# Kernel tuning notes

Hardware: AMD Instinct MI355X
Metric: run time of the kernel (lower is better)

Reference implementation:

```python
import jax, jax.numpy as jnp
import numpy as np


def setup_inputs() -> dict:
    key = jax.random.key(0)
    ks = jax.random.split(key, 9)
    B, S, D, DK, DV = 4, 4096, 1024, 128, 128
    scale = 1.0 / np.sqrt(D)
    return {
        "q": jax.random.normal(ks[0], (B, S, D), jnp.float32),
        "k": jax.random.normal(ks[1], (B, S, D), jnp.float32),
        "v": jax.random.normal(ks[2], (B, S, D), jnp.float32),
        "Wq": jax.random.normal(ks[3], (D, DK), jnp.float32) * scale,
        "bq": jnp.zeros((DK,), jnp.float32),
        "Wk": jax.random.normal(ks[4], (D, DK), jnp.float32) * scale,
        "bk": jnp.zeros((DK,), jnp.float32),
        "Wv": jax.random.normal(ks[5], (D, DV), jnp.float32) * scale,
        "bv": jnp.zeros((DV,), jnp.float32),
    }


def reference(q, k, v, Wq, bq, Wk, bk, Wv, bv):
    # Q/K/V projections (nn.Linear)
    Q = q @ Wq + bq          # [B,S,DK]
    K = k @ Wk + bk          # [B,S,DK]
    V = v @ Wv + bv          # [B,S,DV]
    scale = Q.shape[-1] ** 0.5
    scores = jnp.einsum("bqd,bkd->bqk", Q, K) / scale  # [B,Sq,Sk]
    attn = jax.nn.softmax(scores, axis=-1)
    return jnp.einsum("bqk,bkd->bqd", attn, V)          # [B,Sq,DV]
```

## Files before the change

### kernel.cpp

```cpp
#include <hip/hip_runtime.h>
#include <hip/hip_bf16.h>
#include <cstdint>
#include <cmath>


typedef __bf16 bf16x8 __attribute__((ext_vector_type(8)));
typedef float f32x4 __attribute__((ext_vector_type(4)));
typedef float f32x16 __attribute__((ext_vector_type(16)));

typedef const __attribute__((address_space(1))) unsigned int* gp_t;
typedef __attribute__((address_space(3))) unsigned int* lp_t;

__device__ __forceinline__ unsigned short f2bf(float f) {
  unsigned u = __float_as_uint(f);
  u += 0x7fffu + ((u >> 16) & 1u);
  return (unsigned short)(u >> 16);
}

__device__ __forceinline__ bf16x8 ld_frag(const char* p) {
  uint4 u = *reinterpret_cast<const uint4*>(p);
  return __builtin_bit_cast(bf16x8, u);
}

__device__ __forceinline__ unsigned cvtpk_bf16(float lo, float hi) {
  unsigned r;
  asm("v_cvt_pk_bf16_f32 %0, %1, %2" : "=v"(r) : "v"(lo), "v"(hi));
  return r;
}

__device__ __forceinline__ void pl32swap(unsigned &a, unsigned &b) {
  asm("v_permlane32_swap_b32 %0, %1" : "+v"(a), "+v"(b));
}

__device__ __forceinline__ bf16x8 mk_frag(unsigned w0, unsigned w1, unsigned w2, unsigned w3) {
  uint4 u{w0, w1, w2, w3};
  return __builtin_bit_cast(bf16x8, u);
}

__device__ __forceinline__ float bfhi2f(unsigned u) {
  return __uint_as_float(u & 0xffff0000u);
}
__device__ __forceinline__ float bflo2f(unsigned u) {
  return __uint_as_float(u << 16);
}

#define QSCALE_LOG2E 0.12751744f

__global__ __launch_bounds__(256) void prep_wt_kernel(
    const float* __restrict__ W0, const float* __restrict__ W1, const float* __restrict__ W2,
    unsigned short* __restrict__ T0, unsigned short* __restrict__ T1,
    unsigned short* __restrict__ T2) {
  const int mode = blockIdx.z;
  const float* W = (mode == 0) ? W0 : (mode == 1) ? W1 : W2;
  unsigned short* Wt = (mode == 0) ? T0 : (mode == 1) ? T1 : T2;
  __shared__ float tile[64][65];
  int kt = blockIdx.x, nt = blockIdx.y;
  int tid = threadIdx.x;
  int c = tid & 63;
  int r0 = (tid >> 6) * 16;
#pragma unroll
  for (int i = 0; i < 16; ++i) {
    int r = r0 + i;
    tile[r][c] = W[(size_t)(kt * 64 + r) * 128 + nt * 64 + c];
  }
  __syncthreads();
#pragma unroll
  for (int i = 0; i < 16; ++i) {
    int n = r0 + i;
    Wt[(size_t)(nt * 64 + n) * 1024 + kt * 64 + c] = f2bf(tile[c][n]);
  }
}

__global__ __launch_bounds__(256, 3) void proj_kernel(
    const float* __restrict__ qx, const float* __restrict__ kx, const float* __restrict__ vx,
    const unsigned short* __restrict__ Wtq, const unsigned short* __restrict__ Wtk,
    const unsigned short* __restrict__ Wtv,
    const float* __restrict__ bq, const float* __restrict__ bk, const float* __restrict__ bv,
    unsigned short* __restrict__ Qb, unsigned short* __restrict__ Kb,
    unsigned short* __restrict__ Vtb) {
  const int mode = blockIdx.y;
  const float* x = (mode == 0) ? qx : (mode == 1) ? kx : vx;
  const unsigned short* Wt = (mode == 0) ? Wtq : (mode == 1) ? Wtk : Wtv;
  const float* bias = (mode == 0) ? bq : (mode == 1) ? bk : bv;

  __shared__ __align__(16) char lds[49152];
  char* ldsA = lds;
  char* ldsW = lds + 16384;

  const int tid = threadIdx.x;
  const int lane = tid & 63, wid = tid >> 6;
  const int l15 = lane & 15, hi = lane >> 4;
  const long row0 = (long)blockIdx.x * 64;

  const int a_row0 = tid >> 5;
  const int a_c16  = tid & 31;
  const float* a_src = x + (row0 + a_row0) * 1024 + a_c16 * 4;
  const int a_swz = (a_row0 & 7) << 4;
  const int a_wbyte = (((a_c16 >> 1) * 16) ^ a_swz) + (a_c16 & 1) * 8;

  const char* w_src = (const char*)Wt + (size_t)(tid >> 4) * 2048 +
                      (size_t)((tid & 15) ^ ((tid >> 4) & 7)) * 16;

  f32x4 acc[8];
#pragma unroll
  for (int i = 0; i < 8; ++i) acc[i] = f32x4{0.f, 0.f, 0.f, 0.f};

  const int arow = wid * 16 + l15;
  const int aswzr = (arow & 7) << 4;

#pragma unroll 1
  for (int t = 0; t < 8; ++t) {
    f32x4 av[8];
#pragma unroll
    for (int j = 0; j < 8; ++j)
      av[j] = *reinterpret_cast<const f32x4*>(a_src + t * 128 + j * 8192);
#pragma unroll
    for (int i = 0; i < 8; ++i)
      __builtin_amdgcn_global_load_lds((gp_t)(w_src + (size_t)i * 32768 + t * 256),
                                       (lp_t)(ldsW + i * 4096 + wid * 1024), 16, 0, 0);
#pragma unroll
    for (int j = 0; j < 8; ++j) {
      uint2 wv;
      wv.x = cvtpk_bf16(av[j][0], av[j][1]);
      wv.y = cvtpk_bf16(av[j][2], av[j][3]);
      *reinterpret_cast<uint2*>(ldsA + a_row0 * 256 + j * 2048 + a_wbyte) = wv;
    }
    __syncthreads();

    bf16x8 af[4];
#pragma unroll
    for (int kk = 0; kk < 4; ++kk)
      af[kk] = ld_frag(ldsA + ((arow * 256 + (kk * 4 + hi) * 16) ^ aswzr));
#pragma unroll
    for (int ni = 0; ni < 8; ++ni) {
      int n = ni * 16 + l15;
      int nswz = (n & 7) << 4;
#pragma unroll
      for (int kk = 0; kk < 4; ++kk) {
        bf16x8 wf = ld_frag(ldsW + ((n * 256 + (kk * 4 + hi) * 16) ^ nswz));
        acc[ni] = __builtin_amdgcn_mfma_f32_16x16x32_bf16(af[kk], wf, acc[ni], 0, 0, 0);
      }
    }
    __syncthreads();
  }

#pragma unroll
  for (int ni = 0; ni < 8; ++ni) {
    int n = ni * 16 + l15;
    float bv_ = bias[n];
    long m = row0 + wid * 16 + hi * 4;
    f32x4 a = acc[ni];
    if (mode == 2) {
      int bb = (int)(m >> 12);
      int s = (int)(m & 4095);
      ushort4 pk;
      pk.x = f2bf(a[0] + bv_); pk.y = f2bf(a[1] + bv_);
      pk.z = f2bf(a[2] + bv_); pk.w = f2bf(a[3] + bv_);
      *reinterpret_cast<ushort4*>(Vtb + ((size_t)(bb * 128 + n)) * 4096 + s) = pk;
    } else {
      const float sc = (mode == 0) ? QSCALE_LOG2E : 1.0f;
      unsigned short* outp = (mode == 0) ? Qb : Kb;
      outp[(m + 0) * 128 + n] = f2bf((a[0] + bv_) * sc);
      outp[(m + 1) * 128 + n] = f2bf((a[1] + bv_) * sc);
      outp[(m + 2) * 128 + n] = f2bf((a[2] + bv_) * sc);
      outp[(m + 3) * 128 + n] = f2bf((a[3] + bv_) * sc);
    }
  }
}

template <int TPS>
__global__ __launch_bounds__(256, 2) void attn_kernel(
    const unsigned short* __restrict__ Qb, const unsigned short* __restrict__ Kb,
    const unsigned short* __restrict__ Vtb, unsigned short* __restrict__ Po,
    float* __restrict__ ml) {
  __shared__ __align__(16) char lds[65536];

  const int tid = threadIdx.x;
  const int lane = tid & 63, wid = tid >> 6;
  const int l31 = lane & 31, hi = lane >> 5;
  const int split = blockIdx.y;
  const int b = blockIdx.z;
  const int qbase = blockIdx.x * 128 + wid * 32;
  const size_t growq = (size_t)b * 4096 + qbase + l31;

  const char* kg0 = (const char*)Kb + (size_t)(b * 4096) * 256;
  const char* vg0 = (const char*)Vtb + (size_t)b * 128 * 4096 * 2;
  const int k_row = tid >> 4;
  const int slog  = (tid & 15) ^ (tid >> 4);
  const int v_dv0 = 2 * (tid >> 4) + (slog >> 3);
  const int v_ksl = slog & 7;

#define ATTN_STAGE(KV0, BUF)                                                          \
  {                                                                                   \
    char* kb_ = lds + (BUF) * 16384;                                                  \
    char* vb_ = lds + 32768 + (BUF) * 16384;                                          \
    const char* kgs_ = kg0 + (size_t)(KV0) * 256 + (size_t)k_row * 256 + slog * 16;   \
    const char* vgs_ = vg0 + (size_t)(KV0) * 2 + (size_t)v_dv0 * 8192 + v_ksl * 16;   \
    _Pragma("unroll")                                                                 \
    for (int i = 0; i < 4; ++i)                                                       \
      __builtin_amdgcn_global_load_lds((gp_t)(kgs_ + (size_t)i * 4096),               \
                                       (lp_t)(kb_ + i * 4096 + wid * 1024), 16, 0, 0);\
    _Pragma("unroll")                                                                 \
    for (int i = 0; i < 4; ++i)                                                       \
      __builtin_amdgcn_global_load_lds((gp_t)(vgs_ + (size_t)i * 262144),             \
                                       (lp_t)(vb_ + i * 4096 + wid * 1024), 16, 0, 0);\
  }

  bf16x8 qf[8];
  {
    const unsigned short* qp = Qb + growq * 128 + hi * 8;
#pragma unroll
    for (int kt = 0; kt < 8; ++kt)
      qf[kt] = __builtin_bit_cast(bf16x8, *reinterpret_cast<const uint4*>(qp + kt * 16));
  }

  f32x16 oacc[4];
#pragma unroll
  for (int d = 0; d < 4; ++d)
#pragma unroll
    for (int j = 0; j < 16; ++j) oacc[d][j] = 0.f;
  float mrun = -INFINITY, lrun = 0.f;

  const int t0 = split * TPS, t1 = t0 + TPS;

  ATTN_STAGE(t0 * 64, 0);
  ATTN_STAGE((t0 + 1) * 64, 1);

  const int kswz = l31 & 15;
  const int vjx  = l31 >> 1;
  const int vslb = (l31 & 1) << 3;

#pragma unroll 1
  for (int t = t0; t < t1; ++t) {
    const int buf = (t - t0) & 1;
    if (t < t1 - 1) asm volatile("s_waitcnt vmcnt(8)" ::: "memory");
    else            asm volatile("s_waitcnt vmcnt(0)" ::: "memory");
    __builtin_amdgcn_s_barrier();
    __builtin_amdgcn_sched_barrier(0);
    char* ldsK = lds + buf * 16384;
    char* ldsV = lds + 32768 + buf * 16384;

    f32x16 sc0, sc1;
#pragma unroll
    for (int j = 0; j < 16; ++j) { sc0[j] = 0.f; sc1[j] = 0.f; }
    __builtin_amdgcn_s_setprio(1);
#pragma unroll
    for (int kvb = 0; kvb < 2; ++kvb) {
      int rowoff = (kvb * 32 + l31) * 256;
#pragma unroll
      for (int kt = 0; kt < 8; ++kt) {
        bf16x8 kf = ld_frag(ldsK + rowoff + ((((kt << 1) + hi) ^ kswz) << 4));
        if (kvb == 0) sc0 = __builtin_amdgcn_mfma_f32_32x32x16_bf16(kf, qf[kt], sc0, 0, 0, 0);
        else          sc1 = __builtin_amdgcn_mfma_f32_32x32x16_bf16(kf, qf[kt], sc1, 0, 0, 0);
      }
    }
    __builtin_amdgcn_s_setprio(0);

    float tmx[16];
#pragma unroll
    for (int i = 0; i < 16; ++i) tmx[i] = fmaxf(sc0[i], sc1[i]);
#pragma unroll
    for (int s = 8; s > 0; s >>= 1)
#pragma unroll
      for (int i = 0; i < s; ++i) tmx[i] = fmaxf(tmx[i], tmx[i + s]);
    float mt = tmx[0];
    mt = fmaxf(mt, __shfl_xor(mt, 32));

    if (!__all(mt - mrun <= 8.0f)) {
      float mnew = fmaxf(mrun, mt);
      float scl = exp2f(mrun - mnew);
      mrun = mnew;
      lrun *= scl;
#pragma unroll
      for (int d = 0; d < 4; ++d)
#pragma unroll
        for (int j = 0; j < 16; ++j) oacc[d][j] *= scl;
    }

#pragma unroll
    for (int i = 0; i < 16; ++i) {
      sc0[i] = exp2f(sc0[i] - mrun);
      sc1[i] = exp2f(sc1[i] - mrun);
    }
    float ts[16];
#pragma unroll
    for (int i = 0; i < 16; ++i) ts[i] = sc0[i] + sc1[i];
#pragma unroll
    for (int s = 8; s > 0; s >>= 1)
#pragma unroll
      for (int i = 0; i < s; ++i) ts[i] += ts[i + s];
    float psum = ts[0];
    psum += __shfl_xor(psum, 32);
    lrun += psum;

    bf16x8 pa[4];
#pragma unroll
    for (int c = 0; c < 2; ++c) {
      const f32x16& p = c ? sc1 : sc0;
#pragma unroll
      for (int g = 0; g < 2; ++g) {
        const int base = g * 8;
        unsigned a0 = cvtpk_bf16(p[base + 0], p[base + 1]);
        unsigned b0 = cvtpk_bf16(p[base + 4], p[base + 5]);
        pl32swap(a0, b0);
        unsigned a1 = cvtpk_bf16(p[base + 2], p[base + 3]);
        unsigned b1 = cvtpk_bf16(p[base + 6], p[base + 7]);
        pl32swap(a1, b1);
        pa[c * 2 + g] = mk_frag(a0, a1, b0, b1);
      }
    }

    __builtin_amdgcn_s_setprio(1);
#pragma unroll
    for (int dvb = 0; dvb < 4; ++dvb) {
      int jbase = (dvb * 16 + vjx) * 256;
#pragma unroll
      for (int tt = 0; tt < 4; ++tt) {
        bf16x8 vf = ld_frag(ldsV + jbase + (((vslb + tt * 2 + hi) ^ vjx) << 4));
        oacc[dvb] = __builtin_amdgcn_mfma_f32_32x32x16_bf16(vf, pa[tt], oacc[dvb], 0, 0, 0);
      }
    }
    __builtin_amdgcn_s_setprio(0);

    __builtin_amdgcn_s_barrier();
    __builtin_amdgcn_sched_barrier(0);
    if (t + 2 < t1) ATTN_STAGE((t + 2) * 64, buf);
  }

#undef ATTN_STAGE

  if (hi == 0) {
    float* mlp = ml + (size_t)split * 32768 + growq * 2;
    mlp[0] = mrun; mlp[1] = lrun;
  }

  unsigned short* po = Po + ((size_t)split << 21) + ((size_t)b * 4096 + qbase) * 128;
  char* tbase = lds + wid * 4096;
  for (int dvb = 0; dvb < 4; ++dvb) {
#pragma unroll
    for (int g = 0; g < 4; ++g) {
      float4 w4{oacc[dvb][g * 4 + 0], oacc[dvb][g * 4 + 1],
                oacc[dvb][g * 4 + 2], oacc[dvb][g * 4 + 3]};
      int off = (l31 * 128 + g * 32 + hi * 16) ^ ((l31 & 7) << 4);
      *reinterpret_cast<float4*>(tbase + off) = w4;
    }
    asm volatile("s_waitcnt lgkmcnt(0)" ::: "memory");
    __builtin_amdgcn_sched_barrier(0);
#pragma unroll
    for (int qq = 0; qq < 4; ++qq) {
      int q = qq * 8 + (lane >> 3);
      int off = (q * 128 + (lane & 7) * 16) ^ ((q & 7) << 4);
      float4 r4 = *reinterpret_cast<const float4*>(tbase + off);
      uint2 pk{cvtpk_bf16(r4.x, r4.y), cvtpk_bf16(r4.z, r4.w)};
      *reinterpret_cast<uint2*>(po + (size_t)q * 128 + dvb * 32 + (lane & 7) * 4) = pk;
    }
    asm volatile("s_waitcnt lgkmcnt(0)" ::: "memory");
    __builtin_amdgcn_sched_barrier(0);
  }
}

template <int NS>
__global__ __launch_bounds__(256) void combine_kernel(const unsigned short* __restrict__ Po,
                                                      const float* __restrict__ ml,
                                                      float* __restrict__ out) {
  int idx = blockIdx.x * 256 + threadIdx.x;
  int grow = idx >> 5;
  int c4 = (idx & 31) * 4;
  float m[NS], l[NS];
  float M = -INFINITY;
#pragma unroll
  for (int s = 0; s < NS; ++s) {
    m[s] = ml[(size_t)s * 32768 + grow * 2 + 0];
    l[s] = ml[(size_t)s * 32768 + grow * 2 + 1];
    M = fmaxf(M, m[s]);
  }
  float L = 0.f, w[NS];
#pragma unroll
  for (int s = 0; s < NS; ++s) {
    w[s] = exp2f(m[s] - M);
    L += l[s] * w[s];
  }
  float invL = 1.0f / L;
  float4 acc = {0.f, 0.f, 0.f, 0.f};
#pragma unroll
  for (int s = 0; s < NS; ++s) {
    uint2 pv = *reinterpret_cast<const uint2*>(Po + ((size_t)s << 21) + (size_t)grow * 128 + c4);
    acc.x += bflo2f(pv.x) * w[s];
    acc.y += bfhi2f(pv.x) * w[s];
    acc.z += bflo2f(pv.y) * w[s];
    acc.w += bfhi2f(pv.y) * w[s];
  }
  acc.x *= invL; acc.y *= invL; acc.z *= invL; acc.w *= invL;
  *reinterpret_cast<float4*>(out + (size_t)grow * 128 + c4) = acc;
}

extern "C" void kernel_launch(void* const* d_in, const int* in_sizes, int n_in,
                              void* d_out, int out_size, void* d_ws, size_t ws_size,
                              hipStream_t stream) {
  const float* q  = (const float*)d_in[0];
  const float* k  = (const float*)d_in[1];
  const float* v  = (const float*)d_in[2];
  const float* Wq = (const float*)d_in[3];
  const float* bq = (const float*)d_in[4];
  const float* Wk = (const float*)d_in[5];
  const float* bk = (const float*)d_in[6];
  const float* Wv = (const float*)d_in[7];
  const float* bv = (const float*)d_in[8];
  float* out = (float*)d_out;

  char* ws = (char*)d_ws;
  unsigned short* Qb  = (unsigned short*)(ws);
  unsigned short* Kb  = (unsigned short*)(ws + (4u << 20));
  unsigned short* Vtb = (unsigned short*)(ws + (8u << 20));
  unsigned short* Wtq = (unsigned short*)(ws + (12u << 20));
  unsigned short* Wtk = (unsigned short*)(ws + (12u << 20) + (256u << 10));
  unsigned short* Wtv = (unsigned short*)(ws + (12u << 20) + (512u << 10));

  const size_t base = (size_t)13 << 20;
  const size_t per = ((size_t)4 << 20) + ((size_t)128 << 10);
  int nsplit = 1;
  if (ws_size >= base + 4 * per) nsplit = 4;
  else if (ws_size >= base + 2 * per) nsplit = 2;
  unsigned short* Po = (unsigned short*)(ws + base);
  float* ml = (float*)(ws + base + (size_t)nsplit * ((size_t)4 << 20));

  prep_wt_kernel<<<dim3(16, 2, 3), 256, 0, stream>>>(Wq, Wk, Wv, Wtq, Wtk, Wtv);
  proj_kernel<<<dim3(256, 3), 256, 0, stream>>>(q, k, v, Wtq, Wtk, Wtv, bq, bk, bv, Qb, Kb, Vtb);
  if (nsplit == 4) {
    attn_kernel<16><<<dim3(32, 4, 4), 256, 0, stream>>>(Qb, Kb, Vtb, Po, ml);
    combine_kernel<4><<<2048, 256, 0, stream>>>(Po, ml, out);
  } else if (nsplit == 2) {
    attn_kernel<32><<<dim3(32, 2, 4), 256, 0, stream>>>(Qb, Kb, Vtb, Po, ml);
    combine_kernel<2><<<2048, 256, 0, stream>>>(Po, ml, out);
  } else {
    attn_kernel<64><<<dim3(32, 1, 4), 256, 0, stream>>>(Qb, Kb, Vtb, Po, ml);
    combine_kernel<1><<<2048, 256, 0, stream>>>(Po, ml, out);
  }
}
```

Before: 101.7 us.

## Halve attention KV tile to 32 rows, raise occupancy and split-KV to eight

Shrinks each attention iteration from 64 to 32 KV rows, halving the LDS footprint to 32KB and the score registers. This allows four blocks per CU instead of two. It also adds an 8-way split-KV path, doubling the grid, with a matching combine. The aim is better latency hiding and more parallelism, at the cost of twice as many loop iterations and barriers, plus more partial outputs for the combine kernel to read.

New measurement: 154.9 us. 52.3% more time.

```diff
diff --git a/kernel.cpp b/kernel.cpp
--- a/kernel.cpp
+++ b/kernel.cpp
@@ -169,11 +169,11 @@
 }
 
 template <int TPS>
-__global__ __launch_bounds__(256, 2) void attn_kernel(
+__global__ __launch_bounds__(256, 4) void attn_kernel(
     const unsigned short* __restrict__ Qb, const unsigned short* __restrict__ Kb,
     const unsigned short* __restrict__ Vtb, unsigned short* __restrict__ Po,
     float* __restrict__ ml) {
-  __shared__ __align__(16) char lds[65536];
+  __shared__ __align__(16) char lds[32768];
 
   const int tid = threadIdx.x;
   const int lane = tid & 63, wid = tid >> 6;
@@ -187,22 +187,22 @@
   const char* vg0 = (const char*)Vtb + (size_t)b * 128 * 4096 * 2;
   const int k_row = tid >> 4;
   const int slog  = (tid & 15) ^ (tid >> 4);
-  const int v_dv0 = 2 * (tid >> 4) + (slog >> 3);
-  const int v_ksl = slog & 7;
+  const int v_dv0 = 4 * (tid >> 4) + (slog >> 2);
+  const int v_koff = (slog & 3) * 16;
 
 #define ATTN_STAGE(KV0, BUF)                                                          \
   {                                                                                   \
-    char* kb_ = lds + (BUF) * 16384;                                                  \
-    char* vb_ = lds + 32768 + (BUF) * 16384;                                          \
+    char* kb_ = lds + (BUF) * 8192;                                                   \
+    char* vb_ = lds + 16384 + (BUF) * 8192;                                           \
     const char* kgs_ = kg0 + (size_t)(KV0) * 256 + (size_t)k_row * 256 + slog * 16;   \
-    const char* vgs_ = vg0 + (size_t)(KV0) * 2 + (size_t)v_dv0 * 8192 + v_ksl * 16;   \
+    const char* vgs_ = vg0 + (size_t)(KV0) * 2 + (size_t)v_dv0 * 8192 + v_koff;       \
     _Pragma("unroll")                                                                 \
-    for (int i = 0; i < 4; ++i)                                                       \
+    for (int i = 0; i < 2; ++i)                                                       \
       __builtin_amdgcn_global_load_lds((gp_t)(kgs_ + (size_t)i * 4096),               \
                                        (lp_t)(kb_ + i * 4096 + wid * 1024), 16, 0, 0);\
     _Pragma("unroll")                                                                 \
-    for (int i = 0; i < 4; ++i)                                                       \
-      __builtin_amdgcn_global_load_lds((gp_t)(vgs_ + (size_t)i * 262144),             \
+    for (int i = 0; i < 2; ++i)                                                       \
+      __builtin_amdgcn_global_load_lds((gp_t)(vgs_ + (size_t)i * 524288),             \
                                        (lp_t)(vb_ + i * 4096 + wid * 1024), 16, 0, 0);\
   }
 
@@ -223,44 +223,42 @@
 
   const int t0 = split * TPS, t1 = t0 + TPS;
 
-  ATTN_STAGE(t0 * 64, 0);
-  ATTN_STAGE((t0 + 1) * 64, 1);
+  ATTN_STAGE(t0 * 32, 0);
+  ATTN_STAGE((t0 + 1) * 32, 1);
 
   const int kswz = l31 & 15;
-  const int vjx  = l31 >> 1;
-  const int vslb = (l31 & 1) << 3;
+  const int vjx  = l31 >> 2;
+  const int vslb = (l31 & 3) << 2;
 
 #pragma unroll 1
   for (int t = t0; t < t1; ++t) {
     const int buf = (t - t0) & 1;
-    if (t < t1 - 1) asm volatile("s_waitcnt vmcnt(8)" ::: "memory");
+    if (t < t1 - 1) asm volatile("s_waitcnt vmcnt(4)" ::: "memory");
     else            asm volatile("s_waitcnt vmcnt(0)" ::: "memory");
     __builtin_amdgcn_s_barrier();
     __builtin_amdgcn_sched_barrier(0);
-    char* ldsK = lds + buf * 16384;
-    char* ldsV = lds + 32768 + buf * 16384;
-
-    f32x16 sc0, sc1;
-#pragma unroll
-    for (int j = 0; j < 16; ++j) { sc0[j] = 0.f; sc1[j] = 0.f; }
+    char* ldsK = lds + buf * 8192;
+    char* ldsV = lds + 16384 + buf * 8192;
+
+    f32x16 sc;
+#pragma unroll
+    for (int j = 0; j < 16; ++j) sc[j] = 0.f;
     __builtin_amdgcn_s_setprio(1);
-#pragma unroll
-    for (int kvb = 0; kvb < 2; ++kvb) {
-      int rowoff = (kvb * 32 + l31) * 256;
+    {
+      int rowoff = l31 * 256;
 #pragma unroll
       for (int kt = 0; kt < 8; ++kt) {
         bf16x8 kf = ld_frag(ldsK + rowoff + ((((kt << 1) + hi) ^ kswz) << 4));
-        if (kvb == 0) sc0 = __builtin_amdgcn_mfma_f32_32x32x16_bf16(kf, qf[kt], sc0, 0, 0, 0);
-        else          sc1 = __builtin_amdgcn_mfma_f32_32x32x16_bf16(kf, qf[kt], sc1, 0, 0, 0);
+        sc = __builtin_amdgcn_mfma_f32_32x32x16_bf16(kf, qf[kt], sc, 0, 0, 0);
       }
     }
     __builtin_amdgcn_s_setprio(0);
 
-    float tmx[16];
-#pragma unroll
-    for (int i = 0; i < 16; ++i) tmx[i] = fmaxf(sc0[i], sc1[i]);
-#pragma unroll
-    for (int s = 8; s > 0; s >>= 1)
+    float tmx[8];
+#pragma unroll
+    for (int i = 0; i < 8; ++i) tmx[i] = fmaxf(sc[i], sc[i + 8]);
+#pragma unroll
+    for (int s = 4; s > 0; s >>= 1)
 #pragma unroll
       for (int i = 0; i < s; ++i) tmx[i] = fmaxf(tmx[i], tmx[i + s]);
     float mt = tmx[0];
@@ -278,53 +276,47 @@
     }
 
 #pragma unroll
-    for (int i = 0; i < 16; ++i) {
-      sc0[i] = exp2f(sc0[i] - mrun);
-      sc1[i] = exp2f(sc1[i] - mrun);
-    }
-    float ts[16];
-#pragma unroll
-    for (int i = 0; i < 16; ++i) ts[i] = sc0[i] + sc1[i];
-#pragma unroll
-    for (int s = 8; s > 0; s >>= 1)
+    for (int i = 0; i < 16; ++i) sc[i] = exp2f(sc[i] - mrun);
+    float ts[8];
+#pragma unroll
+    for (int i = 0; i < 8; ++i) ts[i] = sc[i] + sc[i + 8];
+#pragma unroll
+    for (int s = 4; s > 0; s >>= 1)
 #pragma unroll
       for (int i = 0; i < s; ++i) ts[i] += ts[i + s];
     float psum = ts[0];
     psum += __shfl_xor(psum, 32);
     lrun += psum;
 
-    bf16x8 pa[4];
-#pragma unroll
-    for (int c = 0; c < 2; ++c) {
-      const f32x16& p = c ? sc1 : sc0;
-#pragma unroll
-      for (int g = 0; g < 2; ++g) {
-        const int base = g * 8;
-        unsigned a0 = cvtpk_bf16(p[base + 0], p[base + 1]);
-        unsigned b0 = cvtpk_bf16(p[base + 4], p[base + 5]);
-        pl32swap(a0, b0);
-        unsigned a1 = cvtpk_bf16(p[base + 2], p[base + 3]);
-        unsigned b1 = cvtpk_bf16(p[base + 6], p[base + 7]);
-        pl32swap(a1, b1);
-        pa[c * 2 + g] = mk_frag(a0, a1, b0, b1);
-      }
+    bf16x8 pb[2];
+#pragma unroll
+    for (int g = 0; g < 2; ++g) {
+      const int base = g * 8;
+      unsigned a0 = cvtpk_bf16(sc[base + 0], sc[base + 1]);
+      unsigned b0 = cvtpk_bf16(sc[base + 4], sc[base + 5]);
+      pl32swap(a0, b0);
+      unsigned a1 = cvtpk_bf16(sc[base + 2], sc[base + 3]);
+      unsigned b1 = cvtpk_bf16(sc[base + 6], sc[base + 7]);
+      pl32swap(a1, b1);
+      pb[g] = mk_frag(a0, a1, b0, b1);
     }
 
     __builtin_amdgcn_s_setprio(1);
 #pragma unroll
     for (int dvb = 0; dvb < 4; ++dvb) {
-      int jbase = (dvb * 16 + vjx) * 256;
-#pragma unroll
-      for (int tt = 0; tt < 4; ++tt) {
-        bf16x8 vf = ld_frag(ldsV + jbase + (((vslb + tt * 2 + hi) ^ vjx) << 4));
-        oacc[dvb] = __builtin_amdgcn_mfma_f32_32x32x16_bf16(vf, pa[tt], oacc[dvb], 0, 0, 0);
+      int jrow = dvb * 8 + vjx;
+      int jbase = jrow * 256, jx = jrow & 15;
+#pragma unroll
+      for (int tt = 0; tt < 2; ++tt) {
+        bf16x8 vf = ld_frag(ldsV + jbase + (((vslb + tt * 2 + hi) ^ jx) << 4));
+        oacc[dvb] = __builtin_amdgcn_mfma_f32_32x32x16_bf16(vf, pb[tt], oacc[dvb], 0, 0, 0);
       }
     }
     __builtin_amdgcn_s_setprio(0);
 
     __builtin_amdgcn_s_barrier();
     __builtin_amdgcn_sched_barrier(0);
-    if (t + 2 < t1) ATTN_STAGE((t + 2) * 64, buf);
+    if (t + 2 < t1) ATTN_STAGE((t + 2) * 32, buf);
   }
 
 #undef ATTN_STAGE
@@ -419,21 +411,25 @@
   const size_t base = (size_t)13 << 20;
   const size_t per = ((size_t)4 << 20) + ((size_t)128 << 10);
   int nsplit = 1;
-  if (ws_size >= base + 4 * per) nsplit = 4;
+  if (ws_size >= base + 8 * per) nsplit = 8;
+  else if (ws_size >= base + 4 * per) nsplit = 4;
   else if (ws_size >= base + 2 * per) nsplit = 2;
   unsigned short* Po = (unsigned short*)(ws + base);
   float* ml = (float*)(ws + base + (size_t)nsplit * ((size_t)4 << 20));
 
   prep_wt_kernel<<<dim3(16, 2, 3), 256, 0, stream>>>(Wq, Wk, Wv, Wtq, Wtk, Wtv);
   proj_kernel<<<dim3(256, 3), 256, 0, stream>>>(q, k, v, Wtq, Wtk, Wtv, bq, bk, bv, Qb, Kb, Vtb);
-  if (nsplit == 4) {
-    attn_kernel<16><<<dim3(32, 4, 4), 256, 0, stream>>>(Qb, Kb, Vtb, Po, ml);
+  if (nsplit == 8) {
+    attn_kernel<16><<<dim3(32, 8, 4), 256, 0, stream>>>(Qb, Kb, Vtb, Po, ml);
+    combine_kernel<8><<<2048, 256, 0, stream>>>(Po, ml, out);
+  } else if (nsplit == 4) {
+    attn_kernel<32><<<dim3(32, 4, 4), 256, 0, stream>>>(Qb, Kb, Vtb, Po, ml);
     combine_kernel<4><<<2048, 256, 0, stream>>>(Po, ml, out);
   } else if (nsplit == 2) {
-    attn_kernel<32><<<dim3(32, 2, 4), 256, 0, stream>>>(Qb, Kb, Vtb, Po, ml);
+    attn_kernel<64><<<dim3(32, 2, 4), 256, 0, stream>>>(Qb, Kb, Vtb, Po, ml);
     combine_kernel<2><<<2048, 256, 0, stream>>>(Po, ml, out);
   } else {
-    attn_kernel<64><<<dim3(32, 1, 4), 256, 0, stream>>>(Qb, Kb, Vtb, Po, ml);
+    attn_kernel<128><<<dim3(32, 1, 4), 256, 0, stream>>>(Qb, Kb, Vtb, Po, ml);
     combine_kernel<1><<<2048, 256, 0, stream>>>(Po, ml, out);
   }
 }
```
